# Optimization experiments

Hardware: AMD Instinct MI355X
Metric: run time of the kernel (lower is better)

## Reference

```python
import jax, jax.numpy as jnp
import numpy as np
from math import factorial

# ---- module hyperparameters (from init_kwargs) ----
SPECIES = np.array([1, 6, 7, 8], np.int32)
LOW, HIGH, NG, RSWITCH, W, LMAX = 0.0, 6.0, 20, 1.0, 2.0, 2
LWEIGHTS = np.array([1.0, 1.0, 1.0], np.float32)
INVF = [2.0, 2.0, 2.0]


def _angular_tables():
    comps, weights, idx, inv = [], [], [], []
    for i in range(LMAX + 1):
        for k in range(i + 1):
            for m in range(i - k + 1):
                n = i - k - m
                comps.append([n, m, k])
                weights.append(factorial(i) / (factorial(n) * factorial(m) * factorial(k)))
                idx.append(i)
                inv.append(INVF[i])
    return (np.array(comps, np.int32), np.array(weights, np.float32),
            np.array(idx, np.int32), np.array(inv, np.float32))

COMPS, ANGW, ANGIDX, INVFACT = _angular_tables()   # 10 angular components for lmax=2
OFFSETS = np.linspace(LOW, HIGH, NG + 1, dtype=np.float32)[1:]
SQRTPI = np.float32(np.sqrt(np.pi))
NSP = len(SPECIES)
COMBOS = [(i, j) for i in range(NSP) for j in range(i + 1, NSP)]
NMBODY = NSP + len(COMBOS)
FPSIZE = NG * (LMAX + 1) * NMBODY


def _int_pow(x, e):
    # e in {0,1,2}; avoids NaN from pow(negative_base, float_exponent)
    return jnp.where(e == 0, jnp.ones_like(x), jnp.where(e == 1, x, x * x))


def _forward(coordinates, nuclear_charges, natom_counts, neighbours):
    B, N, _ = coordinates.shape
    mask = neighbours >= 0                              # padded slots are -1
    nb = jnp.maximum(neighbours, 0)                     # safe_fill
    bidx = jnp.arange(B)[:, None, None]
    local = coordinates[bidx, nb]                       # [B,N,M,3] neighbour gather
    nbh = coordinates[:, :, None, :] - local
    nbh = jnp.where(mask[..., None], nbh, 1.0)          # keep padded slots finite
    d = jnp.linalg.norm(nbh, axis=3)                    # [B,N,M]
    coeff = mask.astype(coordinates.dtype)
    nbr_z = nuclear_charges[bidx, nb]                   # [B,N,M]

    dsw = (d - RSWITCH) / (HIGH - RSWITCH)
    cut = 1.0 - 6.0 * dsw**5 + 15.0 * dsw**4 - 10.0 * dsw**3
    d2 = d * d
    sigma2 = jnp.log(1.0 + W / d2)
    mu = jnp.log(d / jnp.sqrt(1.0 + W / d2))
    off = jnp.asarray(OFFSETS)
    centered = (jnp.log(off) - mu[..., None]) ** 2      # [B,N,M,G]
    s2 = sigma2[..., None]
    radial = (1.0 / (off * jnp.sqrt(s2) * SQRTPI)) * jnp.exp(-centered / (2.0 * s2)) \
             * cut[..., None] * coeff[..., None]        # [B,N,M,G]

    expo = jnp.asarray(INVFACT + ANGIDX.astype(np.float32))
    inv_scaling = (1.0 / d[..., None]) ** expo * coeff[..., None]   # [B,N,M,A]
    comps = jnp.asarray(COMPS)
    angular = inv_scaling \
        * _int_pow(nbh[..., None, 0], comps[:, 0]) \
        * _int_pow(nbh[..., None, 1], comps[:, 1]) \
        * _int_pow(nbh[..., None, 2], comps[:, 2])      # [B,N,M,A]

    angw = jnp.asarray(ANGW)
    lw = jnp.asarray(LWEIGHTS)
    onehot = jnp.asarray((ANGIDX[:, None] == np.arange(LMAX + 1)[None, :]).astype(np.float32))

    sp_masks = [(nbr_z == int(z)).astype(coordinates.dtype) for z in SPECIES]

    def group_fp(gmask):
        ang = angular * gmask[..., None]
        t = jnp.einsum('bnma,bnmg->bnag', ang, radial)          # sum over neighbours
        orb = angw[None, None, :, None] * (t * t)               # [B,N,A,G]
        elem = jnp.einsum('bnag,al->bnlg', orb, onehot)         # index_add over l
        return lw[None, None, :, None] * elem                   # [B,N,L+1,G]

    fps = [group_fp(m) for m in sp_masks]
    for (i, j) in COMBOS:
        gmask = jnp.maximum(sp_masks[i], sp_masks[j])
        fps.append(group_fp(gmask) - (fps[i] + fps[j]))

    fp = jnp.stack(fps, axis=3)                                 # [B,N,L+1,NMBODY,G]
    atom_mask = (jnp.arange(N)[None, :] < natom_counts[:, None]).astype(coordinates.dtype)
    fp = fp * atom_mask[:, :, None, None, None]
    return fp.reshape(B, N, FPSIZE)


def setup_inputs() -> dict:
    rng = np.random.default_rng(0)
    B, N, M = 128, 128, 64
    box = 13.5
    coords = rng.uniform(0.0, box, (B, N, 3)).astype(np.float32)
    charges = rng.choice(np.array([1, 6, 7, 8], np.int32), size=(B, N)).astype(np.int32)
    counts = rng.integers(96, N + 1, B).astype(np.int32)
    diff = coords[:, :, None, :] - coords[:, None, :, :]
    dist = np.linalg.norm(diff, axis=-1)
    exist = np.arange(N)[None, :] < counts[:, None]
    valid = (dist < HIGH) & (dist > 1e-6) & exist[:, :, None] & exist[:, None, :]
    order = np.argsort(~valid, axis=2, kind='stable')[:, :, :M]
    vmask = np.take_along_axis(valid, order, axis=2)
    neighbours = np.where(vmask, order, -1).astype(np.int32)
    return {
        "coordinates": jnp.asarray(coords),
        "nuclear_charges": jnp.asarray(charges),
        "natom_counts": jnp.asarray(counts),
        "neighbours": jnp.asarray(neighbours),
    }


def reference(coordinates, nuclear_charges, natom_counts, neighbours):
    return _forward(coordinates, nuclear_charges, natom_counts, neighbours)
```

## Files before the change

### kernel.cpp

```cpp
#include <hip/hip_runtime.h>


#define B_   128
#define N_   128
#define M_   64
#define NG_  20
#define NSP_ 4
#define FPSIZE_ 600
#define APB  16
#define NTASK (APB * M_)
#define BLOCK_THREADS (APB * NG_)
#define P1ITER 4

__global__ __launch_bounds__(BLOCK_THREADS)
void gto_fp_kernel(const float* __restrict__ coords,
                   const int*   __restrict__ charges,
                   const int*   __restrict__ counts,
                   const int*   __restrict__ neigh,
                   float*       __restrict__ out)
{
    __shared__ float4 sP[APB][M_ + 1];
    __shared__ float2 sQ[APB][M_ + 1];
    __shared__ int s_cnt[APB][NSP_];
    __shared__ int s_start[APB][NSP_];
    __shared__ int s_pos[APB][NSP_];

    const int tid = threadIdx.x;
    const int blockBase = blockIdx.x * APB;
    const int bidx = blockBase / N_;

    if (tid < APB * NSP_) ((int*)s_cnt)[tid] = 0;
    __syncthreads();

    float4 rP[P1ITER];
    float2 rQ[P1ITER];
    int    rls[P1ITER];
    bool   rv[P1ITER];

#pragma unroll
    for (int it = 0; it < P1ITER; ++it) {
        const int t = tid + it * BLOCK_THREADS;
        bool v = (t < NTASK);
        int la = 0, s = 0;
        float4 P = make_float4(0.f, 0.f, 0.f, 0.f);
        float2 Q = make_float2(0.f, 0.f);
        if (v) {
            la = t >> 6;
            const int m  = t & 63;
            const int atom = blockBase + la;
            const int nb = neigh[atom * M_ + m];
            if (nb < 0) {
                v = false;
            } else {
                const int nidx = bidx * N_ + nb;
                const float dx = coords[atom * 3 + 0] - coords[nidx * 3 + 0];
                const float dy = coords[atom * 3 + 1] - coords[nidx * 3 + 1];
                const float dz = coords[atom * 3 + 2] - coords[nidx * 3 + 2];
                const int   z  = charges[nidx];

                const float d2     = dx * dx + dy * dy + dz * dz;
                const float inv_d  = __builtin_amdgcn_rsqf(d2);
                const float d      = d2 * inv_d;
                const float inv_d2 = inv_d * inv_d;

                const float dsw  = (d - 1.0f) * 0.2f;
                const float dsw2 = dsw * dsw;
                const float cut  = 1.0f - dsw2 * dsw * fmaf(6.0f, dsw2, fmaf(-15.0f, dsw, 10.0f));

                const float sigma2 = __logf(fmaf(2.0f, inv_d2, 1.0f));
                const float mu     = 0.5f * (__logf(d2) - sigma2);
                const float amp    = fmaxf(__builtin_amdgcn_rsqf(sigma2) * cut * inv_d2,
                                           1.0e-30f);

                const float F  = -0.72134752f * __builtin_amdgcn_rcpf(sigma2);
                const float Fm = F * mu;
                const float c0 = F;
                const float c1 = -(Fm + Fm);
                const float c2 = fmaf(Fm, mu, __log2f(amp));

                s = (z == 1) ? 0 : (z - 5);
                P = make_float4(c0, c1, c2, dx * inv_d);
                Q = make_float2(dy * inv_d, dz * inv_d);
                atomicAdd(&s_cnt[la][s], 1);
            }
        }
        rP[it] = P; rQ[it] = Q; rls[it] = (la << 2) | s; rv[it] = v;
    }
    __syncthreads();

    if (tid < APB) {
        const int c0 = s_cnt[tid][0], c1 = s_cnt[tid][1], c2 = s_cnt[tid][2];
        s_start[tid][0] = 0;            s_pos[tid][0] = 0;
        s_start[tid][1] = c0;           s_pos[tid][1] = c0;
        s_start[tid][2] = c0 + c1;      s_pos[tid][2] = c0 + c1;
        s_start[tid][3] = c0 + c1 + c2; s_pos[tid][3] = c0 + c1 + c2;
    }
    __syncthreads();

#pragma unroll
    for (int it = 0; it < P1ITER; ++it) {
        if (rv[it]) {
            const int la = rls[it] >> 2, s = rls[it] & 3;
            const int slot = atomicAdd(&s_pos[la][s], 1);
            sP[la][slot] = rP[it];
            sQ[la][slot] = rQ[it];
        }
    }
    __syncthreads();

    const int g  = tid % NG_;
    const int la = tid / NG_;
    const int atom = blockBase + la;
    const int n = atom % N_;

    const float off         = 0.3f * (float)(g + 1);
    const float lo          = __logf(off);
    const float lo2         = lo * lo;
    const float inv_off_spi = 1.0f / (off * 1.7724538509055159f);

    float T[NSP_][10];
#pragma unroll
    for (int s = 0; s < NSP_; ++s)
#pragma unroll
        for (int a = 0; a < 10; ++a) T[s][a] = 0.0f;

#define BODY(SS, P, Q)                                                        \
    {                                                                         \
        const float rad = __builtin_amdgcn_exp2f(                             \
            fmaf(P.x, lo2, fmaf(P.y, lo, P.z)));                              \
        const float rx = rad * P.w, ry = rad * Q.x, rz = rad * Q.y;           \
        T[SS][0] += rad;                                                      \
        T[SS][1] += rx;  T[SS][2] += ry;  T[SS][3] += rz;                     \
        T[SS][4] = fmaf(rx, P.w, T[SS][4]);                                   \
        T[SS][5] = fmaf(rx, Q.x, T[SS][5]);                                   \
        T[SS][6] = fmaf(ry, Q.x, T[SS][6]);                                   \
        T[SS][7] = fmaf(rx, Q.y, T[SS][7]);                                   \
        T[SS][8] = fmaf(ry, Q.y, T[SS][8]);                                   \
        T[SS][9] = fmaf(rz, Q.y, T[SS][9]);                                   \
    }

#define ACC(SS)                                                               \
    {                                                                         \
        const int e0 = s_start[la][SS];                                       \
        const int e1 = e0 + s_cnt[la][SS];                                    \
        int m = e0;                                                           \
        for (; m + 1 < e1; m += 2) {                                          \
            const float4 Pa = sP[la][m];     const float2 Qa = sQ[la][m];     \
            const float4 Pb = sP[la][m + 1]; const float2 Qb = sQ[la][m + 1]; \
            BODY(SS, Pa, Qa)                                                  \
            BODY(SS, Pb, Qb)                                                  \
        }                                                                     \
        if (m < e1) {                                                         \
            const float4 Pa = sP[la][m]; const float2 Qa = sQ[la][m];         \
            BODY(SS, Pa, Qa)                                                  \
        }                                                                     \
    }
    ACC(0) ACC(1) ACC(2) ACC(3)
#undef ACC
#undef BODY

    const float amask = (n < counts[bidx]) ? 1.0f : 0.0f;
    const float scale = amask * inv_off_spi * inv_off_spi;
    float* op = out + atom * FPSIZE_ + g;

#pragma unroll
    for (int l = 0; l < 3; ++l) {
        const int a0 = (l == 0) ? 0 : (l == 1) ? 1 : 4;
        const int a1 = (l == 0) ? 1 : (l == 1) ? 4 : 10;
#pragma unroll
        for (int s = 0; s < NSP_; ++s) {
            float v = 0.0f;
#pragma unroll
            for (int a = a0; a < a1; ++a) {
                const float w = (a == 5 || a == 7 || a == 8) ? 2.0f : 1.0f;
                v = fmaf(w * T[s][a], T[s][a], v);
            }
            op[(l * 10 + s) * NG_] = scale * v;
        }
        int mb = 4;
#pragma unroll
        for (int i = 0; i < NSP_; ++i) {
#pragma unroll
            for (int j = i + 1; j < NSP_; ++j) {
                float v = 0.0f;
#pragma unroll
                for (int a = a0; a < a1; ++a) {
                    const float w = (a == 5 || a == 7 || a == 8) ? 2.0f : 1.0f;
                    v = fmaf(w * T[i][a], T[j][a], v);
                }
                op[(l * 10 + mb) * NG_] = scale * (2.0f * v);
                ++mb;
            }
        }
    }
}

extern "C" void kernel_launch(void* const* d_in, const int* in_sizes, int n_in,
                              void* d_out, int out_size, void* d_ws, size_t ws_size,
                              hipStream_t stream) {
    const float* coords  = (const float*)d_in[0];
    const int*   charges = (const int*)d_in[1];
    const int*   counts  = (const int*)d_in[2];
    const int*   neigh   = (const int*)d_in[3];
    float*       outp    = (float*)d_out;

    const int blocks = (B_ * N_) / APB;
    gto_fp_kernel<<<blocks, BLOCK_THREADS, 0, stream>>>(coords, charges, counts, neigh, outp);
}
```

Baseline: 83.65 us.

## Replace LDS atomics compaction with wave ballot-based species bucketing

Each wave now handles one atom's 64 neighbours at a time. Species buckets are built with ballot, popcount and mbcnt prefix offsets instead of shared-memory atomic counters and position atomics, which drops two block barriers and all LDS atomics. The accumulation loop is unrolled by four with a scalar tail loop, and launch bounds request 5 blocks per CU. The higher unroll and the occupancy hint may raise register pressure or cause spills.

```diff
diff --git a/kernel.cpp b/kernel.cpp
--- a/kernel.cpp
+++ b/kernel.cpp
@@ -8,11 +8,11 @@
 #define NSP_ 4
 #define FPSIZE_ 600
 #define APB  16
-#define NTASK (APB * M_)
 #define BLOCK_THREADS (APB * NG_)
-#define P1ITER 4
-
-__global__ __launch_bounds__(BLOCK_THREADS)
+#define NWAVE (BLOCK_THREADS / 64)
+#define P1ITER ((APB + NWAVE - 1) / NWAVE)
+
+__global__ __launch_bounds__(BLOCK_THREADS, 5)
 void gto_fp_kernel(const float* __restrict__ coords,
                    const int*   __restrict__ charges,
                    const int*   __restrict__ counts,
@@ -21,37 +21,25 @@
 {
     __shared__ float4 sP[APB][M_ + 1];
     __shared__ float2 sQ[APB][M_ + 1];
-    __shared__ int s_cnt[APB][NSP_];
-    __shared__ int s_start[APB][NSP_];
-    __shared__ int s_pos[APB][NSP_];
-
-    const int tid = threadIdx.x;
+    __shared__ int    s_seg[APB][NSP_ + 1];
+
+    const int tid  = threadIdx.x;
+    const int lane = tid & 63;
+    const int wid  = tid >> 6;
     const int blockBase = blockIdx.x * APB;
     const int bidx = blockBase / N_;
 
-    if (tid < APB * NSP_) ((int*)s_cnt)[tid] = 0;
-    __syncthreads();
-
-    float4 rP[P1ITER];
-    float2 rQ[P1ITER];
-    int    rls[P1ITER];
-    bool   rv[P1ITER];
-
 #pragma unroll
     for (int it = 0; it < P1ITER; ++it) {
-        const int t = tid + it * BLOCK_THREADS;
-        bool v = (t < NTASK);
-        int la = 0, s = 0;
-        float4 P = make_float4(0.f, 0.f, 0.f, 0.f);
-        float2 Q = make_float2(0.f, 0.f);
-        if (v) {
-            la = t >> 6;
-            const int m  = t & 63;
+        const int la = wid + it * NWAVE;
+        if (la < APB) {
             const int atom = blockBase + la;
-            const int nb = neigh[atom * M_ + m];
-            if (nb < 0) {
-                v = false;
-            } else {
+            const int nb = neigh[atom * M_ + lane];
+            bool v = (nb >= 0);
+            int s = 0;
+            float4 P = make_float4(0.f, 0.f, 0.f, 0.f);
+            float2 Q = make_float2(0.f, 0.f);
+            if (v) {
                 const int nidx = bidx * N_ + nb;
                 const float dx = coords[atom * 3 + 0] - coords[nidx * 3 + 0];
                 const float dy = coords[atom * 3 + 1] - coords[nidx * 3 + 1];
@@ -81,29 +69,36 @@
                 s = (z == 1) ? 0 : (z - 5);
                 P = make_float4(c0, c1, c2, dx * inv_d);
                 Q = make_float2(dy * inv_d, dz * inv_d);
-                atomicAdd(&s_cnt[la][s], 1);
-            }
-        }
-        rP[it] = P; rQ[it] = Q; rls[it] = (la << 2) | s; rv[it] = v;
-    }
-    __syncthreads();
-
-    if (tid < APB) {
-        const int c0 = s_cnt[tid][0], c1 = s_cnt[tid][1], c2 = s_cnt[tid][2];
-        s_start[tid][0] = 0;            s_pos[tid][0] = 0;
-        s_start[tid][1] = c0;           s_pos[tid][1] = c0;
-        s_start[tid][2] = c0 + c1;      s_pos[tid][2] = c0 + c1;
-        s_start[tid][3] = c0 + c1 + c2; s_pos[tid][3] = c0 + c1 + c2;
-    }
-    __syncthreads();
-
-#pragma unroll
-    for (int it = 0; it < P1ITER; ++it) {
-        if (rv[it]) {
-            const int la = rls[it] >> 2, s = rls[it] & 3;
-            const int slot = atomicAdd(&s_pos[la][s], 1);
-            sP[la][slot] = rP[it];
-            sQ[la][slot] = rQ[it];
+            }
+            const unsigned long long b0 = __ballot(v && (s == 0));
+            const unsigned long long b1 = __ballot(v && (s == 1));
+            const unsigned long long b2 = __ballot(v && (s == 2));
+            const unsigned long long b3 = __ballot(v && (s == 3));
+            const int c0n = __popcll(b0), c1n = __popcll(b1),
+                      c2n = __popcll(b2), c3n = __popcll(b3);
+            const int o0 = __builtin_amdgcn_mbcnt_hi((unsigned)(b0 >> 32),
+                           __builtin_amdgcn_mbcnt_lo((unsigned)b0, 0u));
+            const int o1 = __builtin_amdgcn_mbcnt_hi((unsigned)(b1 >> 32),
+                           __builtin_amdgcn_mbcnt_lo((unsigned)b1, 0u));
+            const int o2 = __builtin_amdgcn_mbcnt_hi((unsigned)(b2 >> 32),
+                           __builtin_amdgcn_mbcnt_lo((unsigned)b2, 0u));
+            const int o3 = __builtin_amdgcn_mbcnt_hi((unsigned)(b3 >> 32),
+                           __builtin_amdgcn_mbcnt_lo((unsigned)b3, 0u));
+            int slot = o0;
+            slot = (s == 1) ? c0n + o1 : slot;
+            slot = (s == 2) ? c0n + c1n + o2 : slot;
+            slot = (s == 3) ? c0n + c1n + c2n + o3 : slot;
+            if (v) {
+                sP[la][slot] = P;
+                sQ[la][slot] = Q;
+            }
+            if (lane == 0) {
+                s_seg[la][0] = 0;
+                s_seg[la][1] = c0n;
+                s_seg[la][2] = c0n + c1n;
+                s_seg[la][3] = c0n + c1n + c2n;
+                s_seg[la][4] = c0n + c1n + c2n + c3n;
+            }
         }
     }
     __syncthreads();
@@ -141,16 +136,20 @@
 
 #define ACC(SS)                                                               \
     {                                                                         \
-        const int e0 = s_start[la][SS];                                       \
-        const int e1 = e0 + s_cnt[la][SS];                                    \
+        const int e0 = s_seg[la][SS];                                         \
+        const int e1 = s_seg[la][SS + 1];                                     \
         int m = e0;                                                           \
-        for (; m + 1 < e1; m += 2) {                                          \
+        for (; m + 3 < e1; m += 4) {                                          \
             const float4 Pa = sP[la][m];     const float2 Qa = sQ[la][m];     \
             const float4 Pb = sP[la][m + 1]; const float2 Qb = sQ[la][m + 1]; \
+            const float4 Pc = sP[la][m + 2]; const float2 Qc = sQ[la][m + 2]; \
+            const float4 Pd = sP[la][m + 3]; const float2 Qd = sQ[la][m + 3]; \
             BODY(SS, Pa, Qa)                                                  \
             BODY(SS, Pb, Qb)                                                  \
+            BODY(SS, Pc, Qc)                                                  \
+            BODY(SS, Pd, Qd)                                                  \
         }                                                                     \
-        if (m < e1) {                                                         \
+        for (; m < e1; ++m) {                                                 \
             const float4 Pa = sP[la][m]; const float2 Qa = sQ[la][m];         \
             BODY(SS, Pa, Qa)                                                  \
         }                                                                     \
```

Result: slower. 88.19 us (+5.4%).
